# Kernel tuning notes

Hardware: AMD Instinct MI355X
Metric: run time of the kernel (lower is better)

The kernel has to match this reference:

```python
import jax, jax.numpy as jnp
import numpy as np

NUM_HEADS = 16
HIDDEN = 1024
EPS = 1e-5


def _layernorm(x, g, b):
    mu = jnp.mean(x, axis=-1, keepdims=True)
    var = jnp.mean((x - mu) ** 2, axis=-1, keepdims=True)
    return (x - mu) * jax.lax.rsqrt(var + EPS) * g + b


def setup_inputs() -> dict:
    key = jax.random.key(0)
    ks = jax.random.split(key, 10)
    B, S, H = 2, 2048, HIDDEN
    s = 0.02
    d = {
        "X": jax.random.normal(ks[0], (B, S, H), jnp.float32),
        "Wq": jax.random.normal(ks[1], (H, H), jnp.float32) * s,
        "bq": jnp.zeros((H,), jnp.float32),
        "Wk": jax.random.normal(ks[2], (H, H), jnp.float32) * s,
        "bk": jnp.zeros((H,), jnp.float32),
        "Wv": jax.random.normal(ks[3], (H, H), jnp.float32) * s,
        "bv": jnp.zeros((H,), jnp.float32),
        "Wo": jax.random.normal(ks[4], (H, H), jnp.float32) * s,
        "bo": jnp.zeros((H,), jnp.float32),
        "ln1_g": jnp.ones((H,), jnp.float32),
        "ln1_b": jnp.zeros((H,), jnp.float32),
        "Wup": jax.random.normal(ks[5], (4 * H, H), jnp.float32) * s,
        "bup": jnp.zeros((4 * H,), jnp.float32),
        "Wdown": jax.random.normal(ks[6], (H, 4 * H), jnp.float32) * s,
        "bdown": jnp.zeros((H,), jnp.float32),
        "ln2_g": jnp.ones((H,), jnp.float32),
        "ln2_b": jnp.zeros((H,), jnp.float32),
    }
    return d


def reference(X, Wq, bq, Wk, bk, Wv, bv, Wo, bo, ln1_g, ln1_b,
              Wup, bup, Wdown, bdown, ln2_g, ln2_b):
    B, S, H = X.shape
    nh = NUM_HEADS
    hd = H // nh
    # QKV projections -> [B, nh, S, hd]
    q = (X @ Wq.T + bq).reshape(B, S, nh, hd).transpose(0, 2, 1, 3)
    k = (X @ Wk.T + bk).reshape(B, S, nh, hd).transpose(0, 2, 1, 3)
    v = (X @ Wv.T + bv).reshape(B, S, nh, hd).transpose(0, 2, 1, 3)
    scores = jnp.einsum("bhqd,bhkd->bhqk", q, k) / jnp.sqrt(jnp.float32(hd))
    causal = jnp.tril(jnp.ones((S, S), dtype=bool))
    scores = jnp.where(causal, scores, jnp.float32(-1e20))
    att = jax.nn.softmax(scores, axis=-1)  # dropout p=0 (eval)
    mid = jnp.einsum("bhqk,bhkd->bhqd", att, v)  # [B, nh, S, hd]
    mid = mid.transpose(0, 2, 1, 3).reshape(B, S, H)
    att_out = mid @ Wo.T + bo
    h = _layernorm(X + att_out, ln1_g, ln1_b)
    up = jax.nn.relu(h @ Wup.T + bup)
    down = up @ Wdown.T + bdown
    return _layernorm(h + down, ln2_g, ln2_b)
```

## Files before the change

kernel.cpp:

```cpp
#include <hip/hip_runtime.h>

#define B_ 2
#define S_ 2048
#define H_ 1024
#define NH 16
#define HD 64
#define LN_EPS 1e-5f

typedef unsigned short u16;
typedef unsigned int u32;
typedef __attribute__((ext_vector_type(8))) short bf16x8;
typedef __attribute__((ext_vector_type(4))) float f32x4;
typedef __attribute__((ext_vector_type(16))) float f32x16;
typedef __attribute__((ext_vector_type(4))) u32 u32x4;
typedef __attribute__((ext_vector_type(4))) u16 u16x4;

__device__ __forceinline__ u16 f2bf(float f) {
  u32 u = __float_as_uint(f);
  u32 r = (u + 0x7FFFu + ((u >> 16) & 1u)) >> 16;
  return (u16)r;
}
__device__ __forceinline__ float bflo(u32 w) { return __uint_as_float(w << 16); }
__device__ __forceinline__ float bfhi(u32 w) { return __uint_as_float(w & 0xffff0000u); }

__device__ __forceinline__ void gload_lds16(const void* g, void* l) {
  __builtin_amdgcn_global_load_lds(
      (const __attribute__((address_space(1))) void*)(uintptr_t)g,
      (__attribute__((address_space(3))) void*)(uintptr_t)l, 16, 0, 0);
}

__global__ __launch_bounds__(256) void k_cvt(const float* __restrict__ in,
                                             u16* __restrict__ out, int n4) {
  int i = blockIdx.x * 256 + threadIdx.x;
  if (i >= n4) return;
  f32x4 v = ((const f32x4*)in)[i];
  u16x4 o = { f2bf(v[0]), f2bf(v[1]), f2bf(v[2]), f2bf(v[3]) };
  ((u16x4*)out)[i] = o;
}

__global__ __launch_bounds__(256) void k_pack3(const float* __restrict__ a,
                                               const float* __restrict__ b,
                                               const float* __restrict__ c,
                                               float* __restrict__ o) {
  int i = blockIdx.x * 256 + threadIdx.x;
  if (i >= 3 * H_) return;
  o[i] = (i < H_) ? a[i] : (i < 2 * H_ ? b[i - H_] : c[i - 2 * H_]);
}

template<int RELU, int F32OUT, int BF16OUT, int BIAS>
__global__ __launch_bounds__(512, 2) void k_gemm8(const u16* __restrict__ A,
                                                  const u16* __restrict__ W,
                                                  const float* __restrict__ bias,
                                                  float* __restrict__ outf,
                                                  u16* __restrict__ outb,
                                                  int M, int N, int lda, int ldb,
                                                  int Kc, int tilesM) {
  extern __shared__ u16 lds[];
  const int tid = threadIdx.x, lane = tid & 63, wid = tid >> 6;
  const int wr = wid >> 2, wc = wid & 3;
  const int lr = lane & 15, lk = lane >> 4;

  const int nwg = gridDim.x;
  const int bid = blockIdx.x;
  const int lid = (bid & 7) * (nwg >> 3) + (bid >> 3);
  const int ty = lid % tilesM;
  const int txz = lid / tilesM;
  const int tilesN = N >> 8;
  const int tx = txz % tilesN;
  const int kz = txz / tilesN;
  const int row0 = ty << 8, col0 = tx << 8;
  A += (size_t)kz * Kc;
  W += (size_t)kz * Kc;
  const size_t outoff = (size_t)kz * M * N;

  const int NT = Kc >> 6;

  f32x4 acc[8][4];
#pragma unroll
  for (int i = 0; i < 8; ++i)
#pragma unroll
    for (int j = 0; j < 4; ++j) acc[i][j] = (f32x4){0.f, 0.f, 0.f, 0.f};

  const int srow = tid >> 3;
  const int csw8 = ((tid & 7) ^ (srow & 7)) << 3;

  auto stage_ht = [&](int ht) {
    const int t = ht >> 2, sel = ht & 3;
    const int mat = (sel < 2) ? 1 : 0;
    const int hh = sel & 1;
    const u16* g = mat ? W : A;
    const int ld = mat ? ldb : lda;
    const int b0 = mat ? col0 : row0;
    const int kt = t << 6;
    u16* dst = lds + ((t & 1) << 15) + (mat << 14) + (hh << 13) + tid * 8;
#pragma unroll
    for (int j = 0; j < 2; ++j) {
      const int r = (hh << 7) + (j << 6) + srow;
      gload_lds16(g + (size_t)(b0 + r) * ld + kt + csw8, dst + (j << 12));
    }
  };

  union UU { u32x4 u; bf16x8 b; };
  auto ldvec = [&](const u16* base, int r, int c) -> bf16x8 {
    UU x;
    x.u = *(const u32x4*)(base + r * 64 + ((c ^ (r & 7)) << 3));
    return x.b;
  };

#pragma unroll
  for (int i = 0; i < 4; ++i) stage_ht(i);
  asm volatile("s_waitcnt vmcnt(0)" ::: "memory");
  __builtin_amdgcn_s_barrier();

  for (int t = 0; t < NT; ++t) {
    const u16* SA = lds + ((t & 1) << 15);
    const u16* SB = SA + 16384;
#pragma unroll
    for (int ph = 0; ph < 4; ++ph) {
      const int mh = ph >> 1, ks = ph & 1;
      const int c = (ks << 2) + lk;
      bf16x8 bb[4], aa[4];
#pragma unroll
      for (int ni = 0; ni < 4; ++ni)
        bb[ni] = ldvec(SB, (wc << 6) + (ni << 4) + lr, c);
#pragma unroll
      for (int mi = 0; mi < 4; ++mi)
        aa[mi] = ldvec(SA, (wr << 7) + (mh << 6) + (mi << 4) + lr, c);
      if (t + 1 < NT && ph < 2) {
        stage_ht(4 * (t + 1) + 2 * ph);
        stage_ht(4 * (t + 1) + 2 * ph + 1);
      }
      __builtin_amdgcn_s_barrier();
      __builtin_amdgcn_s_setprio(1);
#pragma unroll
      for (int mi = 0; mi < 4; ++mi)
#pragma unroll
        for (int ni = 0; ni < 4; ++ni)
          acc[(mh << 2) + mi][ni] = __builtin_amdgcn_mfma_f32_16x16x32_bf16(
              aa[mi], bb[ni], acc[(mh << 2) + mi][ni], 0, 0, 0);
      __builtin_amdgcn_s_setprio(0);
      if (ph == 3)
        asm volatile("s_waitcnt vmcnt(0)" ::: "memory");
      __builtin_amdgcn_s_barrier();
    }
  }

  float bs[4] = {0.f, 0.f, 0.f, 0.f};
  if (BIAS) {
#pragma unroll
    for (int ni = 0; ni < 4; ++ni)
      bs[ni] = bias[col0 + (wc << 6) + (ni << 4) + lr];
  }
#pragma unroll
  for (int mi = 0; mi < 8; ++mi) {
#pragma unroll
    for (int ni = 0; ni < 4; ++ni) {
#pragma unroll
      for (int r = 0; r < 4; ++r) {
        int row = row0 + (wr << 7) + (mi << 4) + (lk << 2) + r;
        int col = col0 + (wc << 6) + (ni << 4) + lr;
        float v = acc[mi][ni][r] + bs[ni];
        if (RELU) v = fmaxf(v, 0.f);
        if (F32OUT) outf[outoff + (size_t)row * N + col] = v;
        if (BF16OUT) outb[outoff + (size_t)row * N + col] = f2bf(v);
      }
    }
  }
}

template<int RELU, int F32OUT, int BF16OUT>
__global__ __launch_bounds__(256) void k_gemm(const u16* __restrict__ A,
                                              const u16* __restrict__ W,
                                              const float* __restrict__ bias,
                                              float* __restrict__ outf,
                                              u16* __restrict__ outb,
                                              int M, int N, int K) {
  __shared__ u16 As[128 * 64];
  __shared__ u16 Bs[128 * 64];
  const int tid = threadIdx.x;
  const int lane = tid & 63;
  const int wid = tid >> 6;
  const int wm = wid >> 1, wn = wid & 1;
  const int row0 = blockIdx.y * 128, col0 = blockIdx.x * 128;
  const int lr = lane & 15, lk = lane >> 4;
  const int sr = lane >> 3, sc = lane & 7;

  f32x4 acc[4][4];
#pragma unroll
  for (int i = 0; i < 4; ++i)
#pragma unroll
    for (int j = 0; j < 4; ++j) acc[i][j] = (f32x4){0.f, 0.f, 0.f, 0.f};

  for (int kt = 0; kt < K; kt += 64) {
#pragma unroll
    for (int i = 0; i < 4; ++i) {
      const int rbase = 32 * wid + 8 * i;
      const int ldsoff = __builtin_amdgcn_readfirstlane(rbase * 64);
      gload_lds16(A + (size_t)(row0 + rbase + sr) * K + kt + sc * 8, As + ldsoff);
      gload_lds16(W + (size_t)(col0 + rbase + sr) * K + kt + sc * 8, Bs + ldsoff);
    }
    __syncthreads();
#pragma unroll
    for (int ks = 0; ks < 2; ++ks) {
      bf16x8 af[4], bfr[4];
#pragma unroll
      for (int mi = 0; mi < 4; ++mi)
        af[mi] = *(const bf16x8*)(As + (wm * 64 + mi * 16 + lr) * 64 + (ks * 4 + lk) * 8);
#pragma unroll
      for (int ni = 0; ni < 4; ++ni)
        bfr[ni] = *(const bf16x8*)(Bs + (wn * 64 + ni * 16 + lr) * 64 + (ks * 4 + lk) * 8);
#pragma unroll
      for (int mi = 0; mi < 4; ++mi)
#pragma unroll
        for (int ni = 0; ni < 4; ++ni)
          acc[mi][ni] = __builtin_amdgcn_mfma_f32_16x16x32_bf16(af[mi], bfr[ni],
                                                                acc[mi][ni], 0, 0, 0);
    }
    __syncthreads();
  }

#pragma unroll
  for (int mi = 0; mi < 4; ++mi) {
#pragma unroll
    for (int ni = 0; ni < 4; ++ni) {
#pragma unroll
      for (int r = 0; r < 4; ++r) {
        int row = row0 + wm * 64 + mi * 16 + lk * 4 + r;
        int col = col0 + wn * 64 + ni * 16 + lr;
        float v = acc[mi][ni][r] + bias[col];
        if (RELU) v = fmaxf(v, 0.f);
        if (F32OUT) outf[(size_t)row * N + col] = v;
        if (BF16OUT) outb[(size_t)row * N + col] = f2bf(v);
      }
    }
  }
}

__global__ __launch_bounds__(256) void k_vt(const u16* __restrict__ QKV,
                                            u16* __restrict__ vt) {
  __shared__ u16 T[64 * 64];
  const int tid = threadIdx.x;
  const int s0 = blockIdx.x * 64;
  const int bh = blockIdx.y;
  const int b = bh >> 4, h = bh & 15;
#pragma unroll
  for (int p = 0; p < 2; ++p) {
    int id = p * 256 + tid;
    int r = id >> 3, c = id & 7;
    u32x4 v = *(const u32x4*)(QKV + (size_t)(b * S_ + s0 + r) * 3072 + 2048 + h * 64 + c * 8);
    int sw = (r ^ (r >> 3)) & 7;
    *(u32x4*)(T + r * 64 + ((c ^ sw) << 3)) = v;
  }
  __syncthreads();
#pragma unroll
  for (int p = 0; p < 2; ++p) {
    int id = p * 256 + tid;
    int d = id >> 3, cs = id & 7;
    u16 tmp[8];
#pragma unroll
    for (int k = 0; k < 8; ++k) {
      int r = cs * 8 + k;
      int sw = (r ^ (r >> 3)) & 7;
      tmp[k] = T[r * 64 + ((((d >> 3) ^ sw)) << 3) + (d & 7)];
    }
    *(u32x4*)(vt + ((size_t)bh * 64 + d) * 2048 + s0 + cs * 8) = *(const u32x4*)tmp;
  }
}

__global__ __launch_bounds__(256, 3) void k_attn_mfma(const u16* __restrict__ QKV,
                                                      const u16* __restrict__ Vt,
                                                      u16* __restrict__ mid) {
  __shared__ u16 lds[9216];
  u16* Ks = lds;
  u16* Vs = lds + 4096;
  const int tid = threadIdx.x, lane = tid & 63, wid = tid >> 6;
  const int lq = lane & 31, lh = lane >> 5;
  const int qb = (S_ / 128 - 1) - blockIdx.x;
  const int bh = blockIdx.y;
  const int b = bh >> 4, h = bh & 15;
  const int q0w = qb * 128 + wid * 32;
  const int qg = q0w + lq;

  union U { u32x4 u; bf16x8 b; };
  U qf[4];
#pragma unroll
  for (int ks = 0; ks < 4; ++ks) {
    const size_t off = (size_t)(b * S_ + qg) * 3072 + h * HD + ks * 16 + lh * 8;
    u32x4 u = *(const u32x4*)(QKV + off);
    u32x4 s;
#pragma unroll
    for (int t = 0; t < 4; ++t) {
      u32 lo = (u32)f2bf(bflo(u[t]) * 0.125f);
      u32 hi = (u32)f2bf(bfhi(u[t]) * 0.125f);
      s[t] = lo | (hi << 16);
    }
    qf[ks].u = s;
  }

  float m = -1e30f, l = 0.f;
  f32x16 acc[2];
#pragma unroll
  for (int mo = 0; mo < 2; ++mo)
#pragma unroll
    for (int r = 0; r < 16; ++r) acc[mo][r] = 0.f;

  const int nt = qb * 2 + 2;
  for (int kv = 0; kv < nt; ++kv) {
    const int kv0 = kv * 64;
    __syncthreads();
#pragma unroll
    for (int p = 0; p < 2; ++p) {
      int id = p * 256 + tid;
      int r = id >> 3, c = id & 7;
      u32x4 ku = *(const u32x4*)(QKV + (size_t)(b * S_ + kv0 + r) * 3072 + 1024 + h * 64 + c * 8);
      *(u32x4*)(Ks + r * 64 + ((c ^ (r & 7)) << 3)) = ku;
      u32x4 vu = *(const u32x4*)(Vt + ((size_t)bh * 64 + r) * 2048 + kv0 + c * 8);
      *(u32x4*)(Vs + r * 64 + ((c ^ (r & 7)) << 3)) = vu;
    }
    __syncthreads();

    if (kv0 > q0w + 31) continue;

    f32x16 sf[2];
#pragma unroll
    for (int nf = 0; nf < 2; ++nf)
#pragma unroll
      for (int r = 0; r < 16; ++r) sf[nf][r] = 0.f;
#pragma unroll
    for (int ks = 0; ks < 4; ++ks) {
#pragma unroll
      for (int nf = 0; nf < 2; ++nf) {
        int r = nf * 32 + lq;
        int c = ks * 2 + lh;
        U kf;
        kf.u = *(const u32x4*)(Ks + r * 64 + ((c ^ (r & 7)) << 3));
        sf[nf] = __builtin_amdgcn_mfma_f32_32x32x16_bf16(kf.b, qf[ks].b, sf[nf], 0, 0, 0);
      }
    }

    if (kv0 + 63 > q0w) {
#pragma unroll
      for (int nf = 0; nf < 2; ++nf)
#pragma unroll
        for (int r = 0; r < 16; ++r) {
          int kvg = kv0 + nf * 32 + (r & 3) + 8 * (r >> 2) + 4 * lh;
          if (kvg > qg) sf[nf][r] = -1e30f;
        }
    }

    float tm = sf[0][0];
#pragma unroll
    for (int r = 1; r < 16; ++r) tm = fmaxf(tm, sf[0][r]);
#pragma unroll
    for (int r = 0; r < 16; ++r) tm = fmaxf(tm, sf[1][r]);
    tm = fmaxf(tm, __shfl_xor(tm, 32));
    const float mn = fmaxf(m, tm);
    const float corr = __expf(m - mn);
    m = mn;
    float rs = 0.f;
#pragma unroll
    for (int nf = 0; nf < 2; ++nf)
#pragma unroll
      for (int r = 0; r < 16; ++r) {
        float p = __expf(sf[nf][r] - mn);
        sf[nf][r] = p;
        rs += p;
      }
    rs += __shfl_xor(rs, 32);
    l = l * corr + rs;
#pragma unroll
    for (int mo = 0; mo < 2; ++mo)
#pragma unroll
      for (int r = 0; r < 16; ++r) acc[mo][r] *= corr;

    u32 q32[2][8];
#pragma unroll
    for (int nf = 0; nf < 2; ++nf)
#pragma unroll
      for (int i = 0; i < 8; ++i)
        asm("v_cvt_pk_bf16_f32 %0, %1, %2"
            : "=v"(q32[nf][i]) : "v"(sf[nf][2 * i]), "v"(sf[nf][2 * i + 1]));

#pragma unroll
    for (int s = 0; s < 4; ++s) {
      const int nfp = s >> 1, sg = s & 1;
      u32 x = q32[nfp][4 * sg + 0];
      u32 y = q32[nfp][4 * sg + 1];
      u32 z = q32[nfp][4 * sg + 2];
      u32 w = q32[nfp][4 * sg + 3];
      asm("v_permlane32_swap_b32 %0, %1" : "+v"(x), "+v"(z));
      asm("v_permlane32_swap_b32 %0, %1" : "+v"(y), "+v"(w));
      U pb;
      pb.u = (u32x4){x, y, z, w};
#pragma unroll
      for (int mo = 0; mo < 2; ++mo) {
        int r = mo * 32 + lq;
        int c = s * 2 + lh;
        U vv;
        vv.u = *(const u32x4*)(Vs + r * 64 + ((c ^ (r & 7)) << 3));
        acc[mo] = __builtin_amdgcn_mfma_f32_32x32x16_bf16(vv.b, pb.b, acc[mo], 0, 0, 0);
      }
    }
  }

  __syncthreads();
  u16* Ow = lds + wid * (32 * 72);
  const float inv = 1.f / l;
#pragma unroll
  for (int mo = 0; mo < 2; ++mo)
#pragma unroll
    for (int r = 0; r < 16; ++r) {
      int d = mo * 32 + (r & 3) + 8 * (r >> 2) + 4 * lh;
      Ow[lq * 72 + d] = f2bf(acc[mo][r] * inv);
    }
  __asm__ volatile("" ::: "memory");
#pragma unroll
  for (int r4 = 0; r4 < 4; ++r4) {
    int ql = r4 * 8 + (lane >> 3);
    int c = lane & 7;
    u32x4 v = *(const u32x4*)(Ow + ql * 72 + c * 8);
    *(u32x4*)(mid + (size_t)(b * S_ + q0w + ql) * H_ + h * HD + c * 8) = v;
  }
}

template<int BF16OUT>
__global__ __launch_bounds__(256) void k_ln(const float* __restrict__ a,
                                            const float* __restrict__ r,
                                            const float* __restrict__ g,
                                            const float* __restrict__ bb,
                                            float* __restrict__ outf,
                                            u16* __restrict__ outb) {
  __shared__ float red[8];
  const int row = blockIdx.x, tid = threadIdx.x;
  const size_t base = (size_t)row * H_ + tid * 4;
  f32x4 va = *(const f32x4*)(a + base);
  f32x4 vr = *(const f32x4*)(r + base);
  f32x4 t = va + vr;
  float sum = t[0] + t[1] + t[2] + t[3];
#pragma unroll
  for (int msk = 32; msk >= 1; msk >>= 1) sum += __shfl_xor(sum, msk, 64);
  if ((tid & 63) == 0) red[tid >> 6] = sum;
  __syncthreads();
  float mu = (red[0] + red[1] + red[2] + red[3]) * (1.f / H_);
  f32x4 d = t - mu;
  float sq = d[0] * d[0] + d[1] * d[1] + d[2] * d[2] + d[3] * d[3];
#pragma unroll
  for (int msk = 32; msk >= 1; msk >>= 1) sq += __shfl_xor(sq, msk, 64);
  if ((tid & 63) == 0) red[4 + (tid >> 6)] = sq;
  __syncthreads();
  float var = (red[4] + red[5] + red[6] + red[7]) * (1.f / H_);
  float rs = rsqrtf(var + LN_EPS);
  f32x4 gg = *(const f32x4*)(g + tid * 4);
  f32x4 bv = *(const f32x4*)(bb + tid * 4);
  f32x4 o = d * rs * gg + bv;
  *(f32x4*)(outf + base) = o;
  if (BF16OUT) {
    u16x4 ob = { f2bf(o[0]), f2bf(o[1]), f2bf(o[2]), f2bf(o[3]) };
    *(u16x4*)(outb + base) = ob;
  }
}

__global__ __launch_bounds__(256) void k_lnr(const float* __restrict__ a,
                                             const u16* __restrict__ P,
                                             const float* __restrict__ bd,
                                             const float* __restrict__ g,
                                             const float* __restrict__ bb,
                                             float* __restrict__ outf) {
  __shared__ float red[8];
  const int row = blockIdx.x, tid = threadIdx.x;
  const size_t base = (size_t)row * H_ + tid * 4;
  f32x4 t = *(const f32x4*)(a + base);
  f32x4 vb = *(const f32x4*)(bd + tid * 4);
  t += vb;
#pragma unroll
  for (int z = 0; z < 4; ++z) {
    u16x4 p = *(const u16x4*)(P + (size_t)z * ((size_t)B_ * S_ * H_) + base);
#pragma unroll
    for (int e = 0; e < 4; ++e) t[e] += __uint_as_float((u32)p[e] << 16);
  }
  float sum = t[0] + t[1] + t[2] + t[3];
#pragma unroll
  for (int msk = 32; msk >= 1; msk >>= 1) sum += __shfl_xor(sum, msk, 64);
  if ((tid & 63) == 0) red[tid >> 6] = sum;
  __syncthreads();
  float mu = (red[0] + red[1] + red[2] + red[3]) * (1.f / H_);
  f32x4 d = t - mu;
  float sq = d[0] * d[0] + d[1] * d[1] + d[2] * d[2] + d[3] * d[3];
#pragma unroll
  for (int msk = 32; msk >= 1; msk >>= 1) sq += __shfl_xor(sq, msk, 64);
  if ((tid & 63) == 0) red[4 + (tid >> 6)] = sq;
  __syncthreads();
  float var = (red[4] + red[5] + red[6] + red[7]) * (1.f / H_);
  float rs = rsqrtf(var + LN_EPS);
  f32x4 gg = *(const f32x4*)(g + tid * 4);
  f32x4 bv = *(const f32x4*)(bb + tid * 4);
  f32x4 o = d * rs * gg + bv;
  *(f32x4*)(outf + base) = o;
}

extern "C" void kernel_launch(void* const* d_in, const int* in_sizes, int n_in,
                              void* d_out, int out_size, void* d_ws, size_t ws_size,
                              hipStream_t stream) {
  const float* X   = (const float*)d_in[0];
  const float* Wq  = (const float*)d_in[1];
  const float* bq  = (const float*)d_in[2];
  const float* Wk  = (const float*)d_in[3];
  const float* bk  = (const float*)d_in[4];
  const float* Wv  = (const float*)d_in[5];
  const float* bv  = (const float*)d_in[6];
  const float* Wo  = (const float*)d_in[7];
  const float* bo  = (const float*)d_in[8];
  const float* g1  = (const float*)d_in[9];
  const float* b1  = (const float*)d_in[10];
  const float* Wup = (const float*)d_in[11];
  const float* bup = (const float*)d_in[12];
  const float* Wdn = (const float*)d_in[13];
  const float* bdn = (const float*)d_in[14];
  const float* g2  = (const float*)d_in[15];
  const float* b2  = (const float*)d_in[16];
  float* out = (float*)d_out;

  const size_t MS = (size_t)B_ * S_;
  const size_t nX = MS * H_;

  char* ws = (char*)d_ws;
  size_t off = 0;
  auto alloc = [&](size_t bytes) {
    char* p = ws + off;
    off += (bytes + 255) & ~(size_t)255;
    return p;
  };
  u16* Xb    = (u16*)alloc(nX * 2);
  u16* Wqkv  = (u16*)alloc((size_t)3 * H_ * H_ * 2);
  u16* Wob   = (u16*)alloc((size_t)H_ * H_ * 2);
  u16* Wupb  = (u16*)alloc((size_t)4 * H_ * H_ * 2);
  u16* Wdnb  = (u16*)alloc((size_t)4 * H_ * H_ * 2);
  float* bqkv = (float*)alloc(3 * H_ * 4);
  u16* QKVb  = (u16*)alloc(nX * 3 * 2);
  u16* midb  = (u16*)alloc(nX * 2);
  u16* Pbuf  = (u16*)alloc(nX * 4 * 2);
  float* h   = (float*)Xb;
  u16* upb   = QKVb;
  u16* vtb   = Pbuf;
  float* att = (float*)Pbuf;
  u16* hb    = Pbuf + nX * 2;
  u16* P     = Pbuf;

  dim3 blk(256);

  k_cvt<<<dim3(4096), blk, 0, stream>>>(X, Xb, (int)(nX / 4));
  k_cvt<<<dim3(1024), blk, 0, stream>>>(Wq, Wqkv, H_ * H_ / 4);
  k_cvt<<<dim3(1024), blk, 0, stream>>>(Wk, Wqkv + (size_t)H_ * H_, H_ * H_ / 4);
  k_cvt<<<dim3(1024), blk, 0, stream>>>(Wv, Wqkv + (size_t)2 * H_ * H_, H_ * H_ / 4);
  k_cvt<<<dim3(1024), blk, 0, stream>>>(Wo, Wob, H_ * H_ / 4);
  k_cvt<<<dim3(4096), blk, 0, stream>>>(Wup, Wupb, 4 * H_ * H_ / 4);
  k_cvt<<<dim3(4096), blk, 0, stream>>>(Wdn, Wdnb, 4 * H_ * H_ / 4);
  k_pack3<<<dim3(12), blk, 0, stream>>>(bq, bk, bv, bqkv);

  k_gemm8<0, 0, 1, 1><<<dim3(16 * 12), dim3(512), 131072, stream>>>(
      Xb, Wqkv, bqkv, nullptr, QKVb, (int)MS, 3 * H_, H_, H_, H_, 16);

  k_vt<<<dim3(S_ / 64, B_ * NH), blk, 0, stream>>>(QKVb, vtb);

  k_attn_mfma<<<dim3(S_ / 128, B_ * NH), blk, 0, stream>>>(QKVb, vtb, midb);

  k_gemm<0, 1, 0><<<dim3(H_ / 128, MS / 128), blk, 0, stream>>>(
      midb, Wob, bo, att, nullptr, (int)MS, H_, H_);

  k_ln<1><<<dim3(MS), blk, 0, stream>>>(X, att, g1, b1, h, hb);

  k_gemm8<1, 0, 1, 1><<<dim3(16 * 16), dim3(512), 131072, stream>>>(
      hb, Wupb, bup, nullptr, upb, (int)MS, 4 * H_, H_, H_, H_, 16);

  k_gemm8<0, 0, 1, 0><<<dim3(16 * 4 * 4), dim3(512), 131072, stream>>>(
      upb, Wdnb, nullptr, nullptr, P, (int)MS, H_, 4 * H_, 4 * H_, H_, 16);

  k_lnr<<<dim3(MS), blk, 0, stream>>>(h, P, bdn, g2, b2, out);
}
```

Before: 250.1 us.

## Double-buffer attention K/V loads and use split-K gemm8 for output projection

The attention kernel now stages the next K/V tile into a second LDS buffer with direct global-to-LDS loads while computing on the current tile, so there is one barrier per iteration and load latency overlaps compute. The occupancy hint of 3 blocks is dropped and LDS use grows to 32 KB. The output projection moves from the old 128x128 GEMM to the 8-wave gemm8 kernel with a split-K of 2 writing bf16 partials. The first layernorm is merged into a templated residual-LN kernel that sums the partials and adds the bias. Bf16 partials lose some precision compared with the previous fp32 attention output.

```diff
diff --git a/kernel.cpp b/kernel.cpp
--- a/kernel.cpp
+++ b/kernel.cpp
@@ -168,74 +168,6 @@
   }
 }
 
-template<int RELU, int F32OUT, int BF16OUT>
-__global__ __launch_bounds__(256) void k_gemm(const u16* __restrict__ A,
-                                              const u16* __restrict__ W,
-                                              const float* __restrict__ bias,
-                                              float* __restrict__ outf,
-                                              u16* __restrict__ outb,
-                                              int M, int N, int K) {
-  __shared__ u16 As[128 * 64];
-  __shared__ u16 Bs[128 * 64];
-  const int tid = threadIdx.x;
-  const int lane = tid & 63;
-  const int wid = tid >> 6;
-  const int wm = wid >> 1, wn = wid & 1;
-  const int row0 = blockIdx.y * 128, col0 = blockIdx.x * 128;
-  const int lr = lane & 15, lk = lane >> 4;
-  const int sr = lane >> 3, sc = lane & 7;
-
-  f32x4 acc[4][4];
-#pragma unroll
-  for (int i = 0; i < 4; ++i)
-#pragma unroll
-    for (int j = 0; j < 4; ++j) acc[i][j] = (f32x4){0.f, 0.f, 0.f, 0.f};
-
-  for (int kt = 0; kt < K; kt += 64) {
-#pragma unroll
-    for (int i = 0; i < 4; ++i) {
-      const int rbase = 32 * wid + 8 * i;
-      const int ldsoff = __builtin_amdgcn_readfirstlane(rbase * 64);
-      gload_lds16(A + (size_t)(row0 + rbase + sr) * K + kt + sc * 8, As + ldsoff);
-      gload_lds16(W + (size_t)(col0 + rbase + sr) * K + kt + sc * 8, Bs + ldsoff);
-    }
-    __syncthreads();
-#pragma unroll
-    for (int ks = 0; ks < 2; ++ks) {
-      bf16x8 af[4], bfr[4];
-#pragma unroll
-      for (int mi = 0; mi < 4; ++mi)
-        af[mi] = *(const bf16x8*)(As + (wm * 64 + mi * 16 + lr) * 64 + (ks * 4 + lk) * 8);
-#pragma unroll
-      for (int ni = 0; ni < 4; ++ni)
-        bfr[ni] = *(const bf16x8*)(Bs + (wn * 64 + ni * 16 + lr) * 64 + (ks * 4 + lk) * 8);
-#pragma unroll
-      for (int mi = 0; mi < 4; ++mi)
-#pragma unroll
-        for (int ni = 0; ni < 4; ++ni)
-          acc[mi][ni] = __builtin_amdgcn_mfma_f32_16x16x32_bf16(af[mi], bfr[ni],
-                                                                acc[mi][ni], 0, 0, 0);
-    }
-    __syncthreads();
-  }
-
-#pragma unroll
-  for (int mi = 0; mi < 4; ++mi) {
-#pragma unroll
-    for (int ni = 0; ni < 4; ++ni) {
-#pragma unroll
-      for (int r = 0; r < 4; ++r) {
-        int row = row0 + wm * 64 + mi * 16 + lk * 4 + r;
-        int col = col0 + wn * 64 + ni * 16 + lr;
-        float v = acc[mi][ni][r] + bias[col];
-        if (RELU) v = fmaxf(v, 0.f);
-        if (F32OUT) outf[(size_t)row * N + col] = v;
-        if (BF16OUT) outb[(size_t)row * N + col] = f2bf(v);
-      }
-    }
-  }
-}
-
 __global__ __launch_bounds__(256) void k_vt(const u16* __restrict__ QKV,
                                             u16* __restrict__ vt) {
   __shared__ u16 T[64 * 64];
@@ -267,12 +199,10 @@
   }
 }
 
-__global__ __launch_bounds__(256, 3) void k_attn_mfma(const u16* __restrict__ QKV,
-                                                      const u16* __restrict__ Vt,
-                                                      u16* __restrict__ mid) {
-  __shared__ u16 lds[9216];
-  u16* Ks = lds;
-  u16* Vs = lds + 4096;
+__global__ __launch_bounds__(256) void k_attn_mfma(const u16* __restrict__ QKV,
+                                                   const u16* __restrict__ Vt,
+                                                   u16* __restrict__ mid) {
+  __shared__ u16 lds[16384];
   const int tid = threadIdx.x, lane = tid & 63, wid = tid >> 6;
   const int lq = lane & 31, lh = lane >> 5;
   const int qb = (S_ / 128 - 1) - blockIdx.x;
@@ -281,6 +211,22 @@
   const int q0w = qb * 128 + wid * 32;
   const int qg = q0w + lq;
 
+  const int srow = tid >> 3, sc = tid & 7;
+  const int ssw = ((sc ^ (srow & 7)) << 3);
+  const u16* srcK = QKV + (size_t)b * S_ * 3072 + 1024 + h * 64;
+  const u16* srcV = Vt + (size_t)bh * 64 * 2048;
+
+  auto stage = [&](int kv, int slot) {
+    u16* dK = lds + slot * 8192 + tid * 8;
+    u16* dV = dK + 4096;
+    const u16* sk = srcK + (size_t)(kv * 64 + srow) * 3072 + ssw;
+    const u16* sv = srcV + (size_t)srow * 2048 + kv * 64 + ssw;
+    gload_lds16(sk, dK);
+    gload_lds16(sk + (size_t)32 * 3072, dK + 2048);
+    gload_lds16(sv, dV);
+    gload_lds16(sv + (size_t)32 * 2048, dV + 2048);
+  };
+
   union U { u32x4 u; bf16x8 b; };
   U qf[4];
 #pragma unroll
@@ -305,105 +251,106 @@
     for (int r = 0; r < 16; ++r) acc[mo][r] = 0.f;
 
   const int nt = qb * 2 + 2;
+
+  stage(0, 0);
+  asm volatile("s_waitcnt vmcnt(0)" ::: "memory");
+  __builtin_amdgcn_s_barrier();
+
   for (int kv = 0; kv < nt; ++kv) {
     const int kv0 = kv * 64;
-    __syncthreads();
-#pragma unroll
-    for (int p = 0; p < 2; ++p) {
-      int id = p * 256 + tid;
-      int r = id >> 3, c = id & 7;
-      u32x4 ku = *(const u32x4*)(QKV + (size_t)(b * S_ + kv0 + r) * 3072 + 1024 + h * 64 + c * 8);
-      *(u32x4*)(Ks + r * 64 + ((c ^ (r & 7)) << 3)) = ku;
-      u32x4 vu = *(const u32x4*)(Vt + ((size_t)bh * 64 + r) * 2048 + kv0 + c * 8);
-      *(u32x4*)(Vs + r * 64 + ((c ^ (r & 7)) << 3)) = vu;
-    }
-    __syncthreads();
-
-    if (kv0 > q0w + 31) continue;
-
-    f32x16 sf[2];
-#pragma unroll
-    for (int nf = 0; nf < 2; ++nf)
-#pragma unroll
-      for (int r = 0; r < 16; ++r) sf[nf][r] = 0.f;
-#pragma unroll
-    for (int ks = 0; ks < 4; ++ks) {
-#pragma unroll
-      for (int nf = 0; nf < 2; ++nf) {
-        int r = nf * 32 + lq;
-        int c = ks * 2 + lh;
-        U kf;
-        kf.u = *(const u32x4*)(Ks + r * 64 + ((c ^ (r & 7)) << 3));
-        sf[nf] = __builtin_amdgcn_mfma_f32_32x32x16_bf16(kf.b, qf[ks].b, sf[nf], 0, 0, 0);
+    const int cur = kv & 1;
+    if (kv + 1 < nt) stage(kv + 1, cur ^ 1);
+
+    if (kv0 <= q0w + 31) {
+      const u16* Ks = lds + cur * 8192;
+      const u16* Vs = Ks + 4096;
+
+      f32x16 sf[2];
+#pragma unroll
+      for (int nf = 0; nf < 2; ++nf)
+#pragma unroll
+        for (int r = 0; r < 16; ++r) sf[nf][r] = 0.f;
+#pragma unroll
+      for (int ks = 0; ks < 4; ++ks) {
+#pragma unroll
+        for (int nf = 0; nf < 2; ++nf) {
+          int r = nf * 32 + lq;
+          int c = ks * 2 + lh;
+          U kf;
+          kf.u = *(const u32x4*)(Ks + r * 64 + ((c ^ (r & 7)) << 3));
+          sf[nf] = __builtin_amdgcn_mfma_f32_32x32x16_bf16(kf.b, qf[ks].b, sf[nf], 0, 0, 0);
+        }
       }
-    }
-
-    if (kv0 + 63 > q0w) {
+
+      if (kv0 + 63 > q0w) {
+#pragma unroll
+        for (int nf = 0; nf < 2; ++nf)
+#pragma unroll
+          for (int r = 0; r < 16; ++r) {
+            int kvg = kv0 + nf * 32 + (r & 3) + 8 * (r >> 2) + 4 * lh;
+            if (kvg > qg) sf[nf][r] = -1e30f;
+          }
+      }
+
+      float tm = sf[0][0];
+#pragma unroll
+      for (int r = 1; r < 16; ++r) tm = fmaxf(tm, sf[0][r]);
+#pragma unroll
+      for (int r = 0; r < 16; ++r) tm = fmaxf(tm, sf[1][r]);
+      tm = fmaxf(tm, __shfl_xor(tm, 32));
+      const float mn = fmaxf(m, tm);
+      const float corr = __expf(m - mn);
+      m = mn;
+      float rs = 0.f;
 #pragma unroll
       for (int nf = 0; nf < 2; ++nf)
 #pragma unroll
         for (int r = 0; r < 16; ++r) {
-          int kvg = kv0 + nf * 32 + (r & 3) + 8 * (r >> 2) + 4 * lh;
-          if (kvg > qg) sf[nf][r] = -1e30f;
+          float p = __expf(sf[nf][r] - mn);
+          sf[nf][r] = p;
+          rs += p;
         }
-    }
-
-    float tm = sf[0][0];
-#pragma unroll
-    for (int r = 1; r < 16; ++r) tm = fmaxf(tm, sf[0][r]);
-#pragma unroll
-    for (int r = 0; r < 16; ++r) tm = fmaxf(tm, sf[1][r]);
-    tm = fmaxf(tm, __shfl_xor(tm, 32));
-    const float mn = fmaxf(m, tm);
-    const float corr = __expf(m - mn);
-    m = mn;
-    float rs = 0.f;
-#pragma unroll
-    for (int nf = 0; nf < 2; ++nf)
-#pragma unroll
-      for (int r = 0; r < 16; ++r) {
-        float p = __expf(sf[nf][r] - mn);
-        sf[nf][r] = p;
-        rs += p;
+      rs += __shfl_xor(rs, 32);
+      l = l * corr + rs;
+#pragma unroll
+      for (int mo = 0; mo < 2; ++mo)
+#pragma unroll
+        for (int r = 0; r < 16; ++r) acc[mo][r] *= corr;
+
+      u32 q32[2][8];
+#pragma unroll
+      for (int nf = 0; nf < 2; ++nf)
+#pragma unroll
+        for (int i = 0; i < 8; ++i)
+          asm("v_cvt_pk_bf16_f32 %0, %1, %2"
+              : "=v"(q32[nf][i]) : "v"(sf[nf][2 * i]), "v"(sf[nf][2 * i + 1]));
+
+#pragma unroll
+      for (int s = 0; s < 4; ++s) {
+        const int nfp = s >> 1, sg = s & 1;
+        u32 x = q32[nfp][4 * sg + 0];
+        u32 y = q32[nfp][4 * sg + 1];
+        u32 z = q32[nfp][4 * sg + 2];
+        u32 w = q32[nfp][4 * sg + 3];
+        asm("v_permlane32_swap_b32 %0, %1" : "+v"(x), "+v"(z));
+        asm("v_permlane32_swap_b32 %0, %1" : "+v"(y), "+v"(w));
+        U pb;
+        pb.u = (u32x4){x, y, z, w};
+#pragma unroll
+        for (int mo = 0; mo < 2; ++mo) {
+          int r = mo * 32 + lq;
+          int c = s * 2 + lh;
+          U vv;
+          vv.u = *(const u32x4*)(Vs + r * 64 + ((c ^ (r & 7)) << 3));
+          acc[mo] = __builtin_amdgcn_mfma_f32_32x32x16_bf16(vv.b, pb.b, acc[mo], 0, 0, 0);
+        }
       }
-    rs += __shfl_xor(rs, 32);
-    l = l * corr + rs;
-#pragma unroll
-    for (int mo = 0; mo < 2; ++mo)
-#pragma unroll
-      for (int r = 0; r < 16; ++r) acc[mo][r] *= corr;
-
-    u32 q32[2][8];
-#pragma unroll
-    for (int nf = 0; nf < 2; ++nf)
-#pragma unroll
-      for (int i = 0; i < 8; ++i)
-        asm("v_cvt_pk_bf16_f32 %0, %1, %2"
-            : "=v"(q32[nf][i]) : "v"(sf[nf][2 * i]), "v"(sf[nf][2 * i + 1]));
-
-#pragma unroll
-    for (int s = 0; s < 4; ++s) {
-      const int nfp = s >> 1, sg = s & 1;
-      u32 x = q32[nfp][4 * sg + 0];
-      u32 y = q32[nfp][4 * sg + 1];
-      u32 z = q32[nfp][4 * sg + 2];
-      u32 w = q32[nfp][4 * sg + 3];
-      asm("v_permlane32_swap_b32 %0, %1" : "+v"(x), "+v"(z));
-      asm("v_permlane32_swap_b32 %0, %1" : "+v"(y), "+v"(w));
-      U pb;
-      pb.u = (u32x4){x, y, z, w};
-#pragma unroll
-      for (int mo = 0; mo < 2; ++mo) {
-        int r = mo * 32 + lq;
-        int c = s * 2 + lh;
-        U vv;
-        vv.u = *(const u32x4*)(Vs + r * 64 + ((c ^ (r & 7)) << 3));
-        acc[mo] = __builtin_amdgcn_mfma_f32_32x32x16_bf16(vv.b, pb.b, acc[mo], 0, 0, 0);
-      }
-    }
-  }
-
-  __syncthreads();
+    }
+
+    asm volatile("s_waitcnt vmcnt(0)" ::: "memory");
+    __builtin_amdgcn_s_barrier();
+  }
+
   u16* Ow = lds + wid * (32 * 72);
   const float inv = 1.f / l;
 #pragma unroll
@@ -423,19 +370,26 @@
   }
 }
 
-template<int BF16OUT>
-__global__ __launch_bounds__(256) void k_ln(const float* __restrict__ a,
-                                            const float* __restrict__ r,
-                                            const float* __restrict__ g,
-                                            const float* __restrict__ bb,
-                                            float* __restrict__ outf,
-                                            u16* __restrict__ outb) {
+template<int BF16OUT, int NZ>
+__global__ __launch_bounds__(256) void k_lnr(const float* __restrict__ a,
+                                             const u16* __restrict__ P,
+                                             const float* __restrict__ bd,
+                                             const float* __restrict__ g,
+                                             const float* __restrict__ bb,
+                                             float* __restrict__ outf,
+                                             u16* __restrict__ outb) {
   __shared__ float red[8];
   const int row = blockIdx.x, tid = threadIdx.x;
   const size_t base = (size_t)row * H_ + tid * 4;
-  f32x4 va = *(const f32x4*)(a + base);
-  f32x4 vr = *(const f32x4*)(r + base);
-  f32x4 t = va + vr;
+  f32x4 t = *(const f32x4*)(a + base);
+  f32x4 vb = *(const f32x4*)(bd + tid * 4);
+  t += vb;
+#pragma unroll
+  for (int z = 0; z < NZ; ++z) {
+    u16x4 p = *(const u16x4*)(P + (size_t)z * ((size_t)B_ * S_ * H_) + base);
+#pragma unroll
+    for (int e = 0; e < 4; ++e) t[e] += __uint_as_float((u32)p[e] << 16);
+  }
   float sum = t[0] + t[1] + t[2] + t[3];
 #pragma unroll
   for (int msk = 32; msk >= 1; msk >>= 1) sum += __shfl_xor(sum, msk, 64);
@@ -458,44 +412,6 @@
     u16x4 ob = { f2bf(o[0]), f2bf(o[1]), f2bf(o[2]), f2bf(o[3]) };
     *(u16x4*)(outb + base) = ob;
   }
-}
-
-__global__ __launch_bounds__(256) void k_lnr(const float* __restrict__ a,
-                                             const u16* __restrict__ P,
-                                             const float* __restrict__ bd,
-                                             const float* __restrict__ g,
-                                             const float* __restrict__ bb,
-                                             float* __restrict__ outf) {
-  __shared__ float red[8];
-  const int row = blockIdx.x, tid = threadIdx.x;
-  const size_t base = (size_t)row * H_ + tid * 4;
-  f32x4 t = *(const f32x4*)(a + base);
-  f32x4 vb = *(const f32x4*)(bd + tid * 4);
-  t += vb;
-#pragma unroll
-  for (int z = 0; z < 4; ++z) {
-    u16x4 p = *(const u16x4*)(P + (size_t)z * ((size_t)B_ * S_ * H_) + base);
-#pragma unroll
-    for (int e = 0; e < 4; ++e) t[e] += __uint_as_float((u32)p[e] << 16);
-  }
-  float sum = t[0] + t[1] + t[2] + t[3];
-#pragma unroll
-  for (int msk = 32; msk >= 1; msk >>= 1) sum += __shfl_xor(sum, msk, 64);
-  if ((tid & 63) == 0) red[tid >> 6] = sum;
-  __syncthreads();
-  float mu = (red[0] + red[1] + red[2] + red[3]) * (1.f / H_);
-  f32x4 d = t - mu;
-  float sq = d[0] * d[0] + d[1] * d[1] + d[2] * d[2] + d[3] * d[3];
-#pragma unroll
-  for (int msk = 32; msk >= 1; msk >>= 1) sq += __shfl_xor(sq, msk, 64);
-  if ((tid & 63) == 0) red[4 + (tid >> 6)] = sq;
-  __syncthreads();
-  float var = (red[4] + red[5] + red[6] + red[7]) * (1.f / H_);
-  float rs = rsqrtf(var + LN_EPS);
-  f32x4 gg = *(const f32x4*)(g + tid * 4);
-  f32x4 bv = *(const f32x4*)(bb + tid * 4);
-  f32x4 o = d * rs * gg + bv;
-  *(f32x4*)(outf + base) = o;
 }
 
 extern "C" void kernel_launch(void* const* d_in, const int* in_sizes, int n_in,
@@ -542,7 +458,7 @@
   float* h   = (float*)Xb;
   u16* upb   = QKVb;
   u16* vtb   = Pbuf;
-  float* att = (float*)Pbuf;
+  u16* WoP   = Pbuf;
   u16* hb    = Pbuf + nX * 2;
   u16* P     = Pbuf;
 
@@ -564,10 +480,10 @@
 
   k_attn_mfma<<<dim3(S_ / 128, B_ * NH), blk, 0, stream>>>(QKVb, vtb, midb);
 
-  k_gemm<0, 1, 0><<<dim3(H_ / 128, MS / 128), blk, 0, stream>>>(
-      midb, Wob, bo, att, nullptr, (int)MS, H_, H_);
-
-  k_ln<1><<<dim3(MS), blk, 0, stream>>>(X, att, g1, b1, h, hb);
+  k_gemm8<0, 0, 1, 0><<<dim3(16 * 4 * 2), dim3(512), 131072, stream>>>(
+      midb, Wob, nullptr, nullptr, WoP, (int)MS, H_, H_, H_, 512, 16);
+
+  k_lnr<1, 2><<<dim3(MS), blk, 0, stream>>>(X, WoP, bo, g1, b1, h, hb);
 
   k_gemm8<1, 0, 1, 1><<<dim3(16 * 16), dim3(512), 131072, stream>>>(
       hb, Wupb, bup, nullptr, upb, (int)MS, 4 * H_, H_, H_, H_, 16);
@@ -575,5 +491,5 @@
   k_gemm8<0, 0, 1, 0><<<dim3(16 * 4 * 4), dim3(512), 131072, stream>>>(
       upb, Wdnb, nullptr, nullptr, P, (int)MS, H_, 4 * H_, 4 * H_, H_, 16);
 
-  k_lnr<<<dim3(MS), blk, 0, stream>>>(h, P, bdn, g2, b2, out);
-}
+  k_lnr<0, 4><<<dim3(MS), blk, 0, stream>>>(h, P, bdn, g2, b2, out, nullptr);
+}
```

New measurement: 251.1 us. About the same (+0.4%).
